# Kernel optimization log

Measured on AMD Instinct MI355X. Metric: run time of the kernel, lower is better.

## Reference

```python
import jax, jax.numpy as jnp
import numpy as np

N = 8192       # num nodes
D_IN = 256     # in_features
D_OUT = 128    # out_features per head
H = 2          # num_heads
E = 262144     # num edges (avg degree 32)
ALPHA = 0.2    # leaky relu slope


def setup_inputs() -> dict:
    key = jax.random.key(0)
    k1, k2, k3, k4 = jax.random.split(key, 4)
    x = jax.random.normal(k1, (N, D_IN), dtype=jnp.float32)
    # per-head Linear weights: W[h] is [out, in] (y = x @ W.T), a[h] is [2*out]
    W = jax.random.normal(k2, (H, D_OUT, D_IN), dtype=jnp.float32) * (1.0 / np.sqrt(D_IN))
    a = jax.random.normal(k3, (H, 2 * D_OUT), dtype=jnp.float32) * (1.0 / np.sqrt(2 * D_OUT))
    edge_index = jax.random.randint(k4, (2, E), 0, N, dtype=jnp.int32)
    return {"x": x, "W": W, "a": a, "edge_index": edge_index}


def reference(x, W, a, edge_index):
    # h[h,n,d] = W(x) per head
    h = jnp.einsum('nf,hdf->hnd', x, W)
    # a([h_i ; h_j]) decomposes into a_src . h_i + a_dst . h_j
    a_src, a_dst = a[:, :D_OUT], a[:, D_OUT:]
    s_i = jnp.einsum('hnd,hd->hn', h, a_src)
    s_j = jnpp_dummy = None
    s_j = jnp.einsum('hnd,hd->hn', h, a_dst)
    score = s_i[:, :, None] + s_j[:, None, :]  # [H, n, n]
    # dense adjacency mask from edge list
    adj = jnp.zeros((N, N), dtype=jnp.bool_).at[edge_index[0], edge_index[1]].set(True)
    # faithful to original: non-edges set to 0 (NOT -inf) before leaky_relu + softmax
    e = jnp.where(adj[None, :, :], score, jnp.float32(0.0))
    e = jnp.where(e > 0, e, ALPHA * e)  # leaky relu
    att = jax.nn.softmax(e, axis=-1)    # softmax over j (dim=1 of original [n,n])
    out = jnp.einsum('hij,hjd->hid', att, h)  # aggregate: attention @ h
    out = jnp.transpose(out, (1, 0, 2)).reshape(N, H * D_OUT)  # concat heads
    return jax.nn.elu(out)
```

## Files before the change

kernel.cpp:

```cpp
#include <hip/hip_runtime.h>
#include <hip/hip_bf16.h>

#define N_NODES 8192
#define DIN     256
#define DOUT    128
#define NHEAD   2
#define CTOT    256
#define LRELU_A 0.2f
#define CAPN    128

typedef __attribute__((ext_vector_type(8))) short bf16x8;
typedef __attribute__((ext_vector_type(4))) float f32x4;

__device__ __forceinline__ float bf(unsigned short u) {
    return __uint_as_float((unsigned)u << 16);
}
__device__ __forceinline__ float bflo(unsigned u) { return __uint_as_float(u << 16); }
__device__ __forceinline__ float bfhi(unsigned u) { return __uint_as_float(u & 0xffff0000u); }
__device__ __forceinline__ unsigned short f2bf(float f) {
    unsigned u = __float_as_uint(f);
    u = (u + 0x7fffu + ((u >> 16) & 1u)) >> 16;
    return (unsigned short)u;
}
__device__ __forceinline__ unsigned pk(float a, float b) {
    return (unsigned)f2bf(a) | ((unsigned)f2bf(b) << 16);
}

__global__ __launch_bounds__(256) void k_pre(const float* __restrict__ x,
                                             const float* __restrict__ W,
                                             const float* __restrict__ a,
                                             unsigned short* __restrict__ hb16,
                                             float* __restrict__ sp_src,
                                             float* __restrict__ sp_dst,
                                             float* __restrict__ cpart,
                                             int*   __restrict__ cnt) {
    __shared__ unsigned short As[64 * 256];
    __shared__ unsigned short Bs[64 * 256];
    __shared__ float          cpl[4][64];
    int b = blockIdx.x, t = threadIdx.x;

    if (b == 512) {
        int4* c4 = reinterpret_cast<int4*>(cnt);
        #pragma unroll
        for (int u = 0; u < 8; ++u)
            c4[u * 256 + t] = make_int4(0, 0, 0, 0);
        return;
    }

    int bmi = b & 127;
    int bm = bmi * 64;
    int bn = (b >> 7) * 64;
    int wv = t >> 6, lane = t & 63;
    int fr = lane & 15, ksl = lane >> 4;

    #pragma unroll
    for (int i = 0; i < 16; ++i) {
        int idx = i * 256 + t;
        int row = idx >> 6;
        int kq  = (idx & 63) * 4;
        float4 v = *reinterpret_cast<const float4*>(&x[(bm + row) * DIN + kq]);
        int slot = kq >> 3, half = (kq >> 2) & 1;
        *reinterpret_cast<uint2*>(&As[row * 256 + ((slot ^ (row & 7)) << 3) + half * 4]) =
            make_uint2(pk(v.x, v.y), pk(v.z, v.w));
    }
    #pragma unroll
    for (int i = 0; i < 16; ++i) {
        int idx = i * 256 + t;
        int row = idx >> 6;
        int kq  = (idx & 63) * 4;
        float4 v = *reinterpret_cast<const float4*>(&W[(bn + row) * DIN + kq]);
        int slot = kq >> 3, half = (kq >> 2) & 1;
        *reinterpret_cast<uint2*>(&Bs[row * 256 + ((slot ^ (row & 7)) << 3) + half * 4]) =
            make_uint2(pk(v.x, v.y), pk(v.z, v.w));
    }
    __syncthreads();

    f32x4 acc[4] = {};
    #pragma unroll
    for (int ch = 0; ch < 8; ++ch) {
        int s = ch * 4 + ksl;
        int ra = wv * 16 + fr;
        bf16x8 af = *reinterpret_cast<const bf16x8*>(&As[ra * 256 + ((s ^ (ra & 7)) << 3)]);
        #pragma unroll
        for (int fn = 0; fn < 4; ++fn) {
            int rb = fn * 16 + fr;
            bf16x8 bfr = *reinterpret_cast<const bf16x8*>(&Bs[rb * 256 + ((s ^ (rb & 7)) << 3)]);
            acc[fn] = __builtin_amdgcn_mfma_f32_16x16x32_bf16(af, bfr, acc[fn], 0, 0, 0);
        }
    }

    #pragma unroll
    for (int fn = 0; fn < 4; ++fn) {
        int c = bn + fn * 16 + fr;
        int r0 = bm + wv * 16 + ksl * 4;
        #pragma unroll
        for (int r = 0; r < 4; ++r)
            hb16[(size_t)(r0 + r) * CTOT + c] = f2bf(acc[fn][r]);
    }

    #pragma unroll
    for (int fn = 0; fn < 4; ++fn) {
        float s = acc[fn][0] + acc[fn][1] + acc[fn][2] + acc[fn][3];
        s += __shfl_xor(s, 16);
        s += __shfl_xor(s, 32);
        if (ksl == 0) cpl[wv][fn * 16 + fr] = s;
    }
    __syncthreads();
    if (t < 64)
        cpart[bmi * 256 + bn + t] = cpl[0][t] + cpl[1][t] + cpl[2][t] + cpl[3][t];

    int head = (bn >= 128);
    int q    = bn >> 6;
    float as[4], ad[4];
    #pragma unroll
    for (int fn = 0; fn < 4; ++fn) {
        int d = (bn & 127) + fn * 16 + fr;
        as[fn] = a[head * 256 + d];
        ad[fn] = a[head * 256 + 128 + d];
    }
    #pragma unroll
    for (int r = 0; r < 4; ++r) {
        float ps = acc[0][r] * as[0] + acc[1][r] * as[1] + acc[2][r] * as[2] + acc[3][r] * as[3];
        float pd = acc[0][r] * ad[0] + acc[1][r] * ad[1] + acc[2][r] * ad[2] + acc[3][r] * ad[3];
        #pragma unroll
        for (int off = 8; off; off >>= 1) {
            ps += __shfl_xor(ps, off);
            pd += __shfl_xor(pd, off);
        }
        if (fr == 0) {
            int row = bm + wv * 16 + ksl * 4 + r;
            sp_src[q * N_NODES + row] = ps;
            sp_dst[q * N_NODES + row] = pd;
        }
    }
}

__global__ __launch_bounds__(256) void k_mid(const int* __restrict__ ei, int E,
                                             int* __restrict__ cnt,
                                             unsigned short* __restrict__ csr,
                                             const float* __restrict__ sp_src,
                                             const float* __restrict__ sp_dst,
                                             const float* __restrict__ cpart,
                                             float* __restrict__ s_src,
                                             float* __restrict__ s_dst,
                                             float* __restrict__ S_all) {
    int b = blockIdx.x, t = threadIdx.x;

    if (b < 1024) {
        int e = b * 256 + t;
        if (e < E) {
            int src = ei[e];
            int dst = ei[E + e];
            int pos = atomicAdd(&cnt[src], 1);
            if (pos < CAPN)
                csr[(size_t)src * CAPN + pos] = (unsigned short)dst;
        }
        return;
    }
    if (b < 1056) {
        int n = (b - 1024) * 256 + t;
        s_src[n]           = sp_src[0 * N_NODES + n] + sp_src[1 * N_NODES + n];
        s_src[N_NODES + n] = sp_src[2 * N_NODES + n] + sp_src[3 * N_NODES + n];
        s_dst[n]           = sp_dst[0 * N_NODES + n] + sp_dst[1 * N_NODES + n];
        s_dst[N_NODES + n] = sp_dst[2 * N_NODES + n] + sp_dst[3 * N_NODES + n];
        return;
    }

    float s = 0.f;
    #pragma unroll 16
    for (int p = 0; p < 128; ++p)
        s += cpart[p * 256 + t];
    S_all[t] = s;
}

__global__ __launch_bounds__(256) void k_attn(const int* __restrict__ cnt,
                                              const unsigned short* __restrict__ csr,
                                              const float* __restrict__ s_src,
                                              const float* __restrict__ s_dst,
                                              const unsigned short* __restrict__ hb16,
                                              const float* __restrict__ S_all,
                                              float* __restrict__ out) {
    __shared__ unsigned mask[2][256];
    __shared__ float    ewl[2][CAPN];
    __shared__ float    zr[2];
    __shared__ float4   part[4][64];

    int i    = blockIdx.x;
    int t    = threadIdx.x;
    int wv   = t >> 6;
    int lane = t & 63;
    int deg  = cnt[i];
    if (deg > CAPN) deg = CAPN;
    const unsigned short* row = csr + (size_t)i * CAPN;

    if ((wv & 1) == 0) {
        int hp = wv >> 1;
        #pragma unroll
        for (int u = 0; u < 4; ++u)
            mask[hp][u * 64 + lane] = 0u;
        float ssh = s_src[hp * N_NODES + i];
        const float* sdh = s_dst + hp * N_NODES;
        float z = 0.f;
        for (int k = lane; k < deg; k += 64) {
            int j = row[k];
            unsigned bit = 1u << (j & 31);
            unsigned old = atomicOr(&mask[hp][j >> 5], bit);
            float w = 0.f;
            if (!(old & bit)) {
                float v = ssh + sdh[j];
                float e = v > 0.f ? v : LRELU_A * v;
                w = expf(e) - 1.f;
            }
            ewl[hp][k] = w;
            z += w;
        }
        #pragma unroll
        for (int off = 32; off; off >>= 1)
            z += __shfl_xor(z, off);
        if (lane == 0) zr[hp] = (float)N_NODES + z;
    }
    __syncthreads();

    const uint2* hb2 = reinterpret_cast<const uint2*>(hb16);
    bool lo = lane < 32;
    float4 acc = make_float4(0.f, 0.f, 0.f, 0.f);
    int k = wv;
    for (; k + 28 < deg; k += 32) {
        int   jj[8]; float ww[8]; uint2 hv[8];
        #pragma unroll
        for (int u = 0; u < 8; ++u) {
            int kk = k + u * 4;
            jj[u] = row[kk];
            ww[u] = lo ? ewl[0][kk] : ewl[1][kk];
            hv[u] = hb2[jj[u] * 64 + lane];
        }
        #pragma unroll
        for (int u = 0; u < 8; ++u) {
            acc.x = fmaf(ww[u], bflo(hv[u].x), acc.x);
            acc.y = fmaf(ww[u], bfhi(hv[u].x), acc.y);
            acc.z = fmaf(ww[u], bflo(hv[u].y), acc.z);
            acc.w = fmaf(ww[u], bfhi(hv[u].y), acc.w);
        }
    }
    for (; k < deg; k += 4) {
        int j = row[k];
        float w = lo ? ewl[0][k] : ewl[1][k];
        uint2 hv = hb2[j * 64 + lane];
        acc.x = fmaf(w, bflo(hv.x), acc.x);
        acc.y = fmaf(w, bfhi(hv.x), acc.y);
        acc.z = fmaf(w, bflo(hv.y), acc.z);
        acc.w = fmaf(w, bfhi(hv.y), acc.w);
    }
    part[wv][lane] = acc;
    __syncthreads();

    if (t < 64) {
        float4 c0 = part[0][t], c1 = part[1][t], c2 = part[2][t], c3 = part[3][t];
        float4 s;
        s.x = c0.x + c1.x + c2.x + c3.x;
        s.y = c0.y + c1.y + c2.y + c3.y;
        s.z = c0.z + c1.z + c2.z + c3.z;
        s.w = c0.w + c1.w + c2.w + c3.w;
        float4 sa = reinterpret_cast<const float4*>(S_all)[t];
        float rz = 1.f / ((t >= 32) ? zr[1] : zr[0]);
        float4 o;
        o.x = (sa.x + s.x) * rz; o.y = (sa.y + s.y) * rz;
        o.z = (sa.z + s.z) * rz; o.w = (sa.w + s.w) * rz;
        o.x = o.x > 0.f ? o.x : expm1f(o.x);
        o.y = o.y > 0.f ? o.y : expm1f(o.y);
        o.z = o.z > 0.f ? o.z : expm1f(o.z);
        o.w = o.w > 0.f ? o.w : expm1f(o.w);
        reinterpret_cast<float4*>(out)[i * 64 + t] = o;
    }
}

extern "C" void kernel_launch(void* const* d_in, const int* in_sizes, int n_in,
                              void* d_out, int out_size, void* d_ws, size_t ws_size,
                              hipStream_t stream) {
    const float* x  = (const float*)d_in[0];
    const float* W  = (const float*)d_in[1];
    const float* a  = (const float*)d_in[2];
    const int*   ei = (const int*)d_in[3];
    int E = in_sizes[3] / 2;
    float* out = (float*)d_out;

    char* ws = (char*)d_ws;
    size_t off = 0;
    auto alloc = [&](size_t bytes) { char* p = ws + off; off += (bytes + 255) & ~(size_t)255; return p; };
    int*            cnt    = (int*)           alloc((size_t)N_NODES * 4);
    unsigned short* csr    = (unsigned short*)alloc((size_t)N_NODES * CAPN * 2);
    float*          S_all  = (float*)         alloc(CTOT * 4);
    float*          s_src  = (float*)         alloc((size_t)NHEAD * N_NODES * 4);
    float*          s_dst  = (float*)         alloc((size_t)NHEAD * N_NODES * 4);
    unsigned short* hb16   = (unsigned short*)alloc((size_t)N_NODES * CTOT * 2);
    float*          sp_src = (float*)         alloc((size_t)4 * N_NODES * 4);
    float*          sp_dst = (float*)         alloc((size_t)4 * N_NODES * 4);
    float*          cpart  = (float*)         alloc((size_t)128 * 256 * 4);

    k_pre<<<513, 256, 0, stream>>>(x, W, a, hb16, sp_src, sp_dst, cpart, cnt);
    k_mid<<<1057, 256, 0, stream>>>(ei, E, cnt, csr, sp_src, sp_dst, cpart, s_src, s_dst, S_all);
    k_attn<<<N_NODES, 256, 0, stream>>>(cnt, csr, s_src, s_dst, hb16, S_all, out);
}
```

Baseline: 55.37 us.

## Deduplicate edges with global adjacency bitmap and compute weights inline in attention

Edge deduplication moves from a per-block shared-memory bitmask in the attention kernel to a global N×N bit adjacency built with atomicOr during CSR construction, so the CSR holds only unique neighbours. The attention kernel then drops its separate weight pass, the shared weight buffer and one barrier, and computes the leaky-relu exp weights inline in the gather loop. Each lane group reduces its own normaliser partials. In exchange, an 8 MB bitmap must be zeroed every call (2048 extra blocks in the first kernel), scattered global atomics are added, and the exp is now computed redundantly by every lane of the wave.

```diff
diff --git a/kernel.cpp b/kernel.cpp
--- a/kernel.cpp
+++ b/kernel.cpp
@@ -6,6 +6,7 @@
 #define DOUT    128
 #define NHEAD   2
 #define CTOT    256
+#define NWORDS  256
 #define LRELU_A 0.2f
 #define CAPN    128
 
@@ -33,7 +34,8 @@
                                              float* __restrict__ sp_src,
                                              float* __restrict__ sp_dst,
                                              float* __restrict__ cpart,
-                                             int*   __restrict__ cnt) {
+                                             int*   __restrict__ cnt,
+                                             float4* __restrict__ adjp) {
     __shared__ unsigned short As[64 * 256];
     __shared__ unsigned short Bs[64 * 256];
     __shared__ float          cpl[4][64];
@@ -44,6 +46,10 @@
         #pragma unroll
         for (int u = 0; u < 8; ++u)
             c4[u * 256 + t] = make_int4(0, 0, 0, 0);
+        return;
+    }
+    if (b >= 513) {
+        adjp[(size_t)(b - 513) * 256 + t] = make_float4(0.f, 0.f, 0.f, 0.f);
         return;
     }
 
@@ -136,6 +142,7 @@
 }
 
 __global__ __launch_bounds__(256) void k_mid(const int* __restrict__ ei, int E,
+                                             unsigned int* __restrict__ adjw,
                                              int* __restrict__ cnt,
                                              unsigned short* __restrict__ csr,
                                              const float* __restrict__ sp_src,
@@ -151,9 +158,13 @@
         if (e < E) {
             int src = ei[e];
             int dst = ei[E + e];
-            int pos = atomicAdd(&cnt[src], 1);
-            if (pos < CAPN)
-                csr[(size_t)src * CAPN + pos] = (unsigned short)dst;
+            unsigned bit = 1u << (dst & 31);
+            unsigned old = atomicOr(&adjw[(size_t)src * NWORDS + (dst >> 5)], bit);
+            if (!(old & bit)) {
+                int pos = atomicAdd(&cnt[src], 1);
+                if (pos < CAPN)
+                    csr[(size_t)src * CAPN + pos] = (unsigned short)dst;
+            }
         }
         return;
     }
@@ -180,77 +191,63 @@
                                               const unsigned short* __restrict__ hb16,
                                               const float* __restrict__ S_all,
                                               float* __restrict__ out) {
-    __shared__ unsigned mask[2][256];
-    __shared__ float    ewl[2][CAPN];
-    __shared__ float    zr[2];
-    __shared__ float4   part[4][64];
+    __shared__ float  zp[4][2];
+    __shared__ float4 part[4][64];
 
     int i    = blockIdx.x;
     int t    = threadIdx.x;
     int wv   = t >> 6;
     int lane = t & 63;
-    int deg  = cnt[i];
+    bool lo  = lane < 32;
+
+    int deg = cnt[i];
     if (deg > CAPN) deg = CAPN;
     const unsigned short* row = csr + (size_t)i * CAPN;
-
-    if ((wv & 1) == 0) {
-        int hp = wv >> 1;
-        #pragma unroll
-        for (int u = 0; u < 4; ++u)
-            mask[hp][u * 64 + lane] = 0u;
-        float ssh = s_src[hp * N_NODES + i];
-        const float* sdh = s_dst + hp * N_NODES;
-        float z = 0.f;
-        for (int k = lane; k < deg; k += 64) {
-            int j = row[k];
-            unsigned bit = 1u << (j & 31);
-            unsigned old = atomicOr(&mask[hp][j >> 5], bit);
-            float w = 0.f;
-            if (!(old & bit)) {
-                float v = ssh + sdh[j];
-                float e = v > 0.f ? v : LRELU_A * v;
-                w = expf(e) - 1.f;
-            }
-            ewl[hp][k] = w;
-            z += w;
-        }
-        #pragma unroll
-        for (int off = 32; off; off >>= 1)
-            z += __shfl_xor(z, off);
-        if (lane == 0) zr[hp] = (float)N_NODES + z;
-    }
-    __syncthreads();
-
     const uint2* hb2 = reinterpret_cast<const uint2*>(hb16);
-    bool lo = lane < 32;
+
+    float ss = lo ? s_src[i] : s_src[N_NODES + i];
+    const float* sd = s_dst + (lo ? 0 : N_NODES);
+
     float4 acc = make_float4(0.f, 0.f, 0.f, 0.f);
+    float  z   = 0.f;
     int k = wv;
     for (; k + 28 < deg; k += 32) {
-        int   jj[8]; float ww[8]; uint2 hv[8];
+        int jj[8]; uint2 hv[8]; float sv[8];
+        #pragma unroll
+        for (int u = 0; u < 8; ++u)
+            jj[u] = row[k + u * 4];
         #pragma unroll
         for (int u = 0; u < 8; ++u) {
-            int kk = k + u * 4;
-            jj[u] = row[kk];
-            ww[u] = lo ? ewl[0][kk] : ewl[1][kk];
             hv[u] = hb2[jj[u] * 64 + lane];
+            sv[u] = sd[jj[u]];
         }
         #pragma unroll
         for (int u = 0; u < 8; ++u) {
-            acc.x = fmaf(ww[u], bflo(hv[u].x), acc.x);
-            acc.y = fmaf(ww[u], bfhi(hv[u].x), acc.y);
-            acc.z = fmaf(ww[u], bflo(hv[u].y), acc.z);
-            acc.w = fmaf(ww[u], bfhi(hv[u].y), acc.w);
+            float v = ss + sv[u];
+            float e = v > 0.f ? v : LRELU_A * v;
+            float w = expf(e) - 1.f;
+            z += w;
+            acc.x = fmaf(w, bflo(hv[u].x), acc.x);
+            acc.y = fmaf(w, bfhi(hv[u].x), acc.y);
+            acc.z = fmaf(w, bflo(hv[u].y), acc.z);
+            acc.w = fmaf(w, bfhi(hv[u].y), acc.w);
         }
     }
     for (; k < deg; k += 4) {
         int j = row[k];
-        float w = lo ? ewl[0][k] : ewl[1][k];
         uint2 hv = hb2[j * 64 + lane];
+        float v = ss + sd[j];
+        float e = v > 0.f ? v : LRELU_A * v;
+        float w = expf(e) - 1.f;
+        z += w;
         acc.x = fmaf(w, bflo(hv.x), acc.x);
         acc.y = fmaf(w, bfhi(hv.x), acc.y);
         acc.z = fmaf(w, bflo(hv.y), acc.z);
         acc.w = fmaf(w, bfhi(hv.y), acc.w);
     }
+
+    if (lane == 0)  zp[wv][0] = z;
+    if (lane == 32) zp[wv][1] = z;
     part[wv][lane] = acc;
     __syncthreads();
 
@@ -261,8 +258,10 @@
         s.y = c0.y + c1.y + c2.y + c3.y;
         s.z = c0.z + c1.z + c2.z + c3.z;
         s.w = c0.w + c1.w + c2.w + c3.w;
+        int hh = t >> 5;
+        float Z = (float)N_NODES + zp[0][hh] + zp[1][hh] + zp[2][hh] + zp[3][hh];
         float4 sa = reinterpret_cast<const float4*>(S_all)[t];
-        float rz = 1.f / ((t >= 32) ? zr[1] : zr[0]);
+        float rz = 1.f / Z;
         float4 o;
         o.x = (sa.x + s.x) * rz; o.y = (sa.y + s.y) * rz;
         o.z = (sa.z + s.z) * rz; o.w = (sa.w + s.w) * rz;
@@ -287,6 +286,7 @@
     char* ws = (char*)d_ws;
     size_t off = 0;
     auto alloc = [&](size_t bytes) { char* p = ws + off; off += (bytes + 255) & ~(size_t)255; return p; };
+    unsigned int*   adjw   = (unsigned int*)  alloc((size_t)N_NODES * NWORDS * 4);
     int*            cnt    = (int*)           alloc((size_t)N_NODES * 4);
     unsigned short* csr    = (unsigned short*)alloc((size_t)N_NODES * CAPN * 2);
     float*          S_all  = (float*)         alloc(CTOT * 4);
@@ -297,7 +297,7 @@
     float*          sp_dst = (float*)         alloc((size_t)4 * N_NODES * 4);
     float*          cpart  = (float*)         alloc((size_t)128 * 256 * 4);
 
-    k_pre<<<513, 256, 0, stream>>>(x, W, a, hb16, sp_src, sp_dst, cpart, cnt);
-    k_mid<<<1057, 256, 0, stream>>>(ei, E, cnt, csr, sp_src, sp_dst, cpart, s_src, s_dst, S_all);
+    k_pre<<<2561, 256, 0, stream>>>(x, W, a, hb16, sp_src, sp_dst, cpart, cnt, (float4*)adjw);
+    k_mid<<<1057, 256, 0, stream>>>(ei, E, adjw, cnt, csr, sp_src, sp_dst, cpart, s_src, s_dst, S_all);
     k_attn<<<N_NODES, 256, 0, stream>>>(cnt, csr, s_src, s_dst, hb16, S_all, out);
 }
```

Result: slower. 65.22 us (+17.8%).
